# Kernel optimization log

Measured on AMD Instinct MI355X. Metric: run time of the kernel, lower is better.

Reference implementation:

```python
import jax, jax.numpy as jnp
import numpy as np

MAX_PT = 20; N_DIM = 2; OUT_SZ = MAX_PT * N_DIM + 2  # 42
FEAT = 512; HID = 512; B = 2048; NL = 32; H = 8; W = 8
SS_PROB = 0.1; BETA = 2.0


def setup_inputs() -> dict:
    key = jax.random.key(0)
    k = jax.random.split(key, 14)
    s = 0.02
    return {
        "img_features": jax.random.normal(k[0], (B, FEAT, H, W), jnp.float32),
        "ground_truth": jax.random.normal(k[1], (B, NL, MAX_PT * N_DIM), jnp.float32),
        "line_prob": jax.random.randint(k[2], (B, NL), 0, 2, jnp.int32),
        "sample_prob": jax.random.uniform(k[3], (NL, B), jnp.float32),
        "att_w": jax.random.normal(k[4], (FEAT + HID,), jnp.float32) * s,
        "att_b": jax.random.normal(k[5], (1,), jnp.float32) * s,
        "gru_w_ih": jax.random.normal(k[6], (3 * HID, FEAT + OUT_SZ), jnp.float32) * s,
        "gru_w_hh": jax.random.normal(k[7], (3 * HID, HID), jnp.float32) * s,
        "gru_b_ih": jax.random.normal(k[8], (3 * HID,), jnp.float32) * s,
        "gru_b_hh": jax.random.normal(k[9], (3 * HID,), jnp.float32) * s,
        "lin1_w": jax.random.normal(k[10], (512, HID), jnp.float32) * s,
        "lin1_b": jax.random.normal(k[11], (512,), jnp.float32) * s,
        "lin2_w": jax.random.normal(k[12], (OUT_SZ, 512), jnp.float32) * s,
        "lin2_b": jax.random.normal(k[13], (OUT_SZ,), jnp.float32) * s,
        "n_lines": NL,
    }


def reference(img_features, ground_truth, line_prob, sample_prob, att_w, att_b,
              gru_w_ih, gru_w_hh, gru_b_ih, gru_b_hh,
              lin1_w, lin1_b, lin2_w, lin2_b, n_lines):
    b, c, h, w = img_features.shape
    hw = h * w
    feat_flat = img_features.reshape(b, c, hw)                     # [B,C,HW]
    # attention branch uses a detached copy of the image features (and hidden)
    img_det = jax.lax.stop_gradient(feat_flat)
    img_logit = jnp.einsum('bcs,c->bs', img_det, att_w[:c])        # image half of 1x1 conv, constant over steps
    w_hid = att_w[c:]

    # scheduled-sampling GT input for step idx uses line idx-1; step 0 uses zeros (previous_output init)
    p = line_prob.astype(jnp.float32)[:, :, None]                  # [B,NL,1]
    ss_gt = jnp.concatenate([ground_truth, 1.0 - p, p], axis=-1)   # [B,NL,OUT]
    ss_gt = jnp.concatenate([jnp.zeros_like(ss_gt[:, :1]), ss_gt[:, :n_lines - 1]], axis=1)
    ss_gt = jnp.swapaxes(ss_gt, 0, 1)                              # [NL,B,OUT]
    use_prev = (sample_prob < SS_PROB).at[0].set(True)             # [NL,B]; step 0 always uses prev (zeros)

    def step(carry, xs):
        h_t, prev = carry
        gt_t, up_t = xs
        ss = jax.lax.stop_gradient(jnp.where(up_t[:, None], prev, gt_t))  # [B,OUT]
        hid_logit = jax.lax.stop_gradient(h_t) @ w_hid                    # [B] hidden half of 1x1 conv (detached)
        att = jax.nn.softmax(img_logit + hid_logit[:, None] + att_b[0], axis=1) * BETA  # [B,HW]
        att_feat = jnp.einsum('bcs,bs->bc', feat_flat, att)               # attention-pooled feature [B,C]
        x = jnp.concatenate([att_feat, ss], axis=1)                       # [B, C+OUT]
        # torch GRU cell: gates ordered r, z, n
        gi = x @ gru_w_ih.T + gru_b_ih
        gh = h_t @ gru_w_hh.T + gru_b_hh
        ir, iz, inn = jnp.split(gi, 3, axis=1)
        hr, hz, hn = jnp.split(gh, 3, axis=1)
        r = jax.nn.sigmoid(ir + hr)
        z = jax.nn.sigmoid(iz + hz)
        n = jnp.tanh(inn + r * hn)
        h_new = (1.0 - z) * n + z * h_t
        o = jax.nn.relu(h_new) @ lin1_w.T + lin1_b
        o = jax.nn.relu(o) @ lin2_w.T + lin2_b                            # [B,OUT]
        return (h_new, o), o

    h0 = jnp.zeros((b, gru_w_hh.shape[1]), img_features.dtype)
    o0 = jnp.zeros((b, lin2_w.shape[0]), img_features.dtype)
    _, outs = jax.lax.scan(step, (h0, o0), (ss_gt, use_prev))
    outs = jnp.swapaxes(outs, 0, 1)                                # [B,NL,OUT]
    npos = outs.shape[-1] - 2
    point_pos = outs[..., :npos]                                   # [B,NL,max_point*n_dim]
    line_out = jax.nn.softmax(outs[..., npos:].reshape(-1, 2), axis=1)  # [B*NL,2]
    return point_pos, line_out
```

## Files before the change

kernel.cpp:

```cpp
#include <hip/hip_runtime.h>
#include <hip/hip_bf16.h>
#include <cstdint>

#define B 2048
#define NL 32
#define FEAT 512
#define HID 512
#define HW 64
#define OUTSZ 42
#define G3 1536
#define LDIH 554
#define MB 16
#define NBLK (B/MB)
#define LDX 584
#define LDH 520
#define CPS 72
#define CHW 16384

typedef __bf16 bf16x8 __attribute__((ext_vector_type(8)));
typedef unsigned short u16x8 __attribute__((ext_vector_type(8)));
typedef float f32x4 __attribute__((ext_vector_type(4)));
typedef __hip_bfloat16 bf16_t;

#define MFMA(a,b,c) __builtin_amdgcn_mfma_f32_16x16x32_bf16(a,b,c,0,0,0)

#define WAITV4() asm volatile("s_waitcnt vmcnt(4)" ::: "memory")
#define PHASE_SYNC() do {                                            \
    asm volatile("s_waitcnt lgkmcnt(0)" ::: "memory");               \
    __builtin_amdgcn_s_barrier();                                    \
  } while (0)
#define PHASE_SYNC_V0() do {                                         \
    asm volatile("s_waitcnt vmcnt(0) lgkmcnt(0)" ::: "memory");      \
    __builtin_amdgcn_s_barrier();                                    \
  } while (0)

static __device__ __forceinline__ float sigmoidf_(float x){ return 1.f/(1.f+__expf(-x)); }

static __device__ __forceinline__ void gld16(const bf16_t* g, bf16_t* l){
  __builtin_amdgcn_global_load_lds(
      (const __attribute__((address_space(1))) void*)g,
      (__attribute__((address_space(3))) void*)l, 16, 0, 0);
}

__global__ __launch_bounds__(256) void prep4_kernel(
    const float* __restrict__ w_ih, const float* __restrict__ w_hh,
    const float* __restrict__ lin1_w, const float* __restrict__ lin2_w,
    const float* __restrict__ b_ih, const float* __restrict__ b_hh,
    bf16_t* __restrict__ sA, bf16_t* __restrict__ sB, bf16_t* __restrict__ sC,
    bf16_t* __restrict__ w_ssn, bf16_t* __restrict__ w_ih512b,
    float* __restrict__ bias_comb){
  const int NA = 54*CHW, NB2 = 16*CHW, NC2 = 2*CHW, NS = 512*64, NI = G3*512;
  const int total = NA+NB2+NC2+NS+NI+G3;
  for (int idx = blockIdx.x*256 + threadIdx.x; idx < total; idx += gridDim.x*256){
    int i = idx;
    if (i < NA){
      int c = i/CHW, r2 = i%CHW, rp = r2>>5, kk = r2&31, gq = kk>>3, e = kk&7;
      int k0 = c/3, g = c%3;
      int half = gq ^ ((rp>>1)&3);
      int orow = g*512 + rp;
      int k = k0*32 + half*8 + e;
      float v = (k < 512) ? w_hh[orow*512 + k]
              : ((k < 512+OUTSZ && g < 2) ? w_ih[(size_t)orow*LDIH + k] : 0.f);
      sA[i] = __float2bfloat16(v);
    } else if ((i -= NA) < NB2){
      int c = i/CHW, r2 = i%CHW, rp = r2>>5, kk = r2&31, gq = kk>>3, e = kk&7;
      int half = gq ^ ((rp>>1)&3);
      sB[i] = __float2bfloat16(lin1_w[rp*512 + c*32 + half*8 + e]);
    } else if ((i -= NB2) < NC2){
      int n = i/CHW, r2 = i%CHW, j = r2>>8, kk = r2&255, s = kk>>3, e = kk&7;
      int g = s ^ (j & 7);
      int k = n*256 + g*8 + e;
      float v = (j < OUTSZ) ? lin2_w[j*512 + k] : 0.f;
      sC[i] = __float2bfloat16(v);
    } else if ((i -= NC2) < NS){
      int j = i>>6, k = i&63;
      float v = (k < OUTSZ) ? w_ih[(size_t)(1024+j)*LDIH + 512 + k] : 0.f;
      w_ssn[i] = __float2bfloat16(v);
    } else if ((i -= NS) < NI){
      int r = i>>9, c = i&511;
      w_ih512b[i] = __float2bfloat16(w_ih[(size_t)r*LDIH + c]);
    } else {
      int j = i - NI;
      bias_comb[j] = b_ih[j] + (j < 1024 ? b_hh[j] : 0.f);
    }
  }
}

__global__ __launch_bounds__(256) void att_kernel(const float* __restrict__ feat,
                                                  const float* __restrict__ att_w,
                                                  bf16_t* __restrict__ att_feat){
  int b = blockIdx.x;
  const float* fb = feat + (size_t)b * FEAT * HW;
  __shared__ float part[4][64];
  __shared__ float attv[64];
  int t = threadIdx.x;
  int s = t & 63, q = t >> 6;
  float acc = 0.f;
  for (int c = q*128; c < q*128 + 128; ++c)
    acc = fmaf(fb[c*HW + s], att_w[c], acc);
  part[q][s] = acc;
  __syncthreads();
  if (t < 64){
    float v = part[0][t] + part[1][t] + part[2][t] + part[3][t];
    float m = v;
    for (int o = 32; o > 0; o >>= 1) m = fmaxf(m, __shfl_xor(m, o));
    float e = __expf(v - m);
    float ssum = e;
    for (int o = 32; o > 0; o >>= 1) ssum += __shfl_xor(ssum, o);
    attv[t] = e / ssum * 2.0f;
  }
  __syncthreads();
  for (int c = t; c < FEAT; c += 256){
    const float4* row = (const float4*)(fb + c*HW);
    float a2 = 0.f;
    #pragma unroll
    for (int k = 0; k < 16; ++k){
      float4 v4 = row[k];
      a2 = fmaf(v4.x, attv[k*4+0], a2);
      a2 = fmaf(v4.y, attv[k*4+1], a2);
      a2 = fmaf(v4.z, attv[k*4+2], a2);
      a2 = fmaf(v4.w, attv[k*4+3], a2);
    }
    att_feat[(size_t)b*FEAT + c] = __float2bfloat16(a2);
  }
}

__global__ __launch_bounds__(256) void gemm_mfma(const bf16_t* __restrict__ A,
                                                 const bf16_t* __restrict__ W,
                                                 const float* __restrict__ bias,
                                                 float* __restrict__ C,
                                                 int K, int lda, int ldw, int ldc){
  const int tid = threadIdx.x;
  const int w = tid >> 6, lane = tid & 63;
  const int r = lane & 15, half = lane >> 4;
  const int m_base = blockIdx.y * 64;
  const int n_base = blockIdx.x * 64 + w * 16;
  const bf16_t* Ap = A + (size_t)(m_base + r)*lda + half*8;
  const bf16_t* Wp = W + (size_t)(n_base + r)*ldw + half*8;
  f32x4 acc[4] = {};
  for (int k0 = 0; k0 < K; k0 += 32){
    bf16x8 bfrag = *(const bf16x8*)(Wp + k0);
    #pragma unroll
    for (int i = 0; i < 4; ++i){
      bf16x8 afrag = *(const bf16x8*)(Ap + (size_t)i*16*lda + k0);
      acc[i] = MFMA(afrag, bfrag, acc[i]);
    }
  }
  const float bv = bias ? bias[n_base + r] : 0.f;
  #pragma unroll
  for (int i = 0; i < 4; ++i)
    #pragma unroll
    for (int q = 0; q < 4; ++q)
      C[(size_t)(m_base + i*16 + half*4 + q)*ldc + n_base + r] = acc[i][q] + bv;
}

__global__ __launch_bounds__(512, 2) void mega13_kernel(
    const float* __restrict__ gi_base,
    const bf16_t* __restrict__ sA,
    const bf16_t* __restrict__ sB,
    const bf16_t* __restrict__ sC,
    const bf16_t* __restrict__ w_ssn,
    const float* __restrict__ lin1_b,
    const float* __restrict__ lin2_b,
    const float* __restrict__ b_hh,
    const float* __restrict__ gt,
    const int* __restrict__ line_prob,
    const float* __restrict__ sample_prob,
    float* __restrict__ out){
  __shared__ bf16_t ring[3*CHW];
  __shared__ bf16_t lds_x[MB][LDX];
  __shared__ bf16_t o1s[MB][LDH];
  const int tid = threadIdx.x;
  const int wv = tid >> 6, l = tid & 63;
  const int lr = l & 15, half = l >> 4;
  const int m0 = blockIdx.x * MB;
  const int colbase = wv * 64;
  const int rowoff = (colbase + lr)*32 + (half ^ ((lr >> 1) & 3))*8;

  for (int i = tid; i < MB*LDX/2; i += 512) ((uint32_t*)lds_x)[i] = 0u;

  float gir[4][4], giz[4][4], gin_[4][4];
  #pragma unroll
  for (int ti = 0; ti < 4; ++ti)
    #pragma unroll
    for (int q = 0; q < 4; ++q){
      const float* gp = gi_base + (size_t)(m0 + half*4 + q)*G3 + colbase + ti*16 + lr;
      gir[ti][q]  = gp[0];
      giz[ti][q]  = gp[512];
      gin_[ti][q] = gp[1024];
    }
  float bhn[4], lb1[4];
  #pragma unroll
  for (int ti = 0; ti < 4; ++ti){
    bhn[ti] = b_hh[1024 + colbase + ti*16 + lr];
    lb1[ti] = lin1_b[colbase + ti*16 + lr];
  }
  const int j3 = wv*16 + lr;
  const float b2c = (wv < 3 && j3 < OUTSZ) ? lin2_b[j3] : 0.f;
  bf16x8 sfr[4][2];
  #pragma unroll
  for (int ti = 0; ti < 4; ++ti)
    #pragma unroll
    for (int ks = 0; ks < 2; ++ks)
      sfr[ti][ks] = *(const bf16x8*)(w_ssn + (size_t)(colbase + ti*16 + lr)*64 + ks*32 + half*8);

  float hp[4][4] = {};

  auto issue = [&](uint32_t g){
    const bf16_t* src = sA;
    if (g < (uint32_t)NL*CPS){
      uint32_t c = g % CPS;
      src = (c < 54) ? sA + (size_t)c*CHW
          : (c < 70) ? sB + (size_t)(c-54)*CHW
                     : sC + (size_t)(c-70)*CHW;
    }
    const int off = wv*2048 + l*8;
    const bf16_t* s = src + off;
    bf16_t* dst = ring + (g % 3)*CHW + off;
    #pragma unroll
    for (int i = 0; i < 4; ++i)
      gld16(s + i*512, dst + i*512);
  };

  __syncthreads();
  uint32_t gc = 0;
  issue(0); issue(1);

  #pragma unroll 1
  for (int t = 0; t < NL; ++t){
    f32x4 accA[3][4] = {};
    #pragma unroll 1
    for (int k0 = 0; k0 < 18; ++k0){
      bf16x8 a = *(const bf16x8*)&lds_x[lr][k0*32 + half*8];
      #pragma unroll
      for (int g = 0; g < 3; ++g){
        WAITV4();
        issue(gc + 2);
        const bf16_t* S = ring + (gc % 3)*CHW;
        #pragma unroll
        for (int ti = 0; ti < 4; ++ti){
          bf16x8 bf = *(const bf16x8*)&S[rowoff + ti*512];
          accA[g][ti] = MFMA(a, bf, accA[g][ti]);
        }
        ++gc;
      }
    }

    f32x4 accS[4] = {};
    #pragma unroll
    for (int ks = 0; ks < 2; ++ks){
      bf16x8 a2 = *(const bf16x8*)&lds_x[lr][512 + ks*32 + half*8];
      #pragma unroll
      for (int ti = 0; ti < 4; ++ti)
        accS[ti] = MFMA(a2, sfr[ti][ks], accS[ti]);
    }
    PHASE_SYNC();

    #pragma unroll
    for (int ti = 0; ti < 4; ++ti)
      #pragma unroll
      for (int q = 0; q < 4; ++q){
        float ir = accA[0][ti][q] + gir[ti][q];
        float iz = accA[1][ti][q] + giz[ti][q];
        float hn = accA[2][ti][q] + bhn[ti];
        float gn = gin_[ti][q] + accS[ti][q];
        float r = sigmoidf_(ir);
        float z = sigmoidf_(iz);
        float n = tanhf(gn + r*hn);
        float hv = (1.f - z)*n + z*hp[ti][q];
        hp[ti][q] = hv;
        lds_x[half*4 + q][colbase + ti*16 + lr] = __float2bfloat16(hv);
      }
    PHASE_SYNC();

    f32x4 accB[4] = {};
    #pragma unroll 1
    for (int cb = 0; cb < 16; ++cb){
      WAITV4();
      issue(gc + 2);
      union { u16x8 u; bf16x8 b; } va;
      va.u = *(const u16x8*)&lds_x[lr][cb*32 + half*8];
      #pragma unroll
      for (int e = 0; e < 8; ++e)
        if (va.u[e] & 0x8000) va.u[e] = 0;
      const bf16_t* S = ring + (gc % 3)*CHW;
      #pragma unroll
      for (int ti = 0; ti < 4; ++ti){
        bf16x8 bf = *(const bf16x8*)&S[rowoff + ti*512];
        accB[ti] = MFMA(va.b, bf, accB[ti]);
      }
      ++gc;
    }
    #pragma unroll
    for (int ti = 0; ti < 4; ++ti)
      #pragma unroll
      for (int q = 0; q < 4; ++q)
        o1s[half*4 + q][colbase + ti*16 + lr] =
            __float2bfloat16(fmaxf(accB[ti][q] + lb1[ti], 0.f));
    PHASE_SYNC_V0();

    f32x4 accC = {};
    #pragma unroll
    for (int n = 0; n < 2; ++n){
      if (wv < 3){
        const bf16_t* S = ring + (gc % 3)*CHW;
        #pragma unroll
        for (int k0 = 0; k0 < 8; ++k0){
          bf16x8 a = *(const bf16x8*)&o1s[lr][(n*8 + k0)*32 + half*8];
          int sg = (k0*4 + half) ^ (j3 & 7);
          bf16x8 bf = *(const bf16x8*)&S[j3*256 + sg*8];
          accC = MFMA(a, bf, accC);
        }
      }
      ++gc;
    }
    if (wv < 3){
      #pragma unroll
      for (int q = 0; q < 4; ++q){
        float val = accC[q] + b2c;
        int row = half*4 + q;
        int bm = m0 + row;
        if (j3 < 40){
          out[((size_t)bm*NL + t)*40 + j3] = val;
        } else if (j3 < 42){
          float other = __shfl_xor(val, 1);
          float mx = fmaxf(val, other);
          float e0 = __expf(val - mx), e1 = __expf(other - mx);
          out[(size_t)B*NL*40 + ((size_t)bm*NL + t)*2 + (j3 - 40)] = e0/(e0 + e1);
        }
        if (t + 1 < NL && j3 < OUTSZ){
          bool up = sample_prob[(size_t)(t+1)*B + bm] < 0.1f;
          float gtv;
          if (j3 < 40) gtv = gt[((size_t)bm*NL + t)*40 + j3];
          else {
            float pv = (float)line_prob[bm*NL + t];
            gtv = (j3 == 40) ? 1.f - pv : pv;
          }
          lds_x[row][512 + j3] = __float2bfloat16(up ? val : gtv);
        }
      }
    }
    PHASE_SYNC();
    issue(gc);
    issue(gc + 1);
  }
}

extern "C" void kernel_launch(void* const* d_in, const int* in_sizes, int n_in,
                              void* d_out, int out_size, void* d_ws, size_t ws_size,
                              hipStream_t stream) {
  const float* img         = (const float*)d_in[0];
  const float* gt          = (const float*)d_in[1];
  const int*   line_prob   = (const int*)d_in[2];
  const float* sample_prob = (const float*)d_in[3];
  const float* att_w       = (const float*)d_in[4];
  const float* w_ih        = (const float*)d_in[6];
  const float* w_hh        = (const float*)d_in[7];
  const float* b_ih        = (const float*)d_in[8];
  const float* b_hh        = (const float*)d_in[9];
  const float* lin1_w      = (const float*)d_in[10];
  const float* lin1_b      = (const float*)d_in[11];
  const float* lin2_w      = (const float*)d_in[12];
  const float* lin2_b      = (const float*)d_in[13];
  float* out = (float*)d_out;

  char* p = (char*)d_ws;
  auto alloc = [&](size_t bytes){ void* q = p; p += (bytes + 255) & ~(size_t)255; return q; };
  float*  gi_base   = (float*)alloc((size_t)B*G3*4);
  bf16_t* att_bf    = (bf16_t*)alloc((size_t)B*FEAT*2);
  bf16_t* sA        = (bf16_t*)alloc((size_t)54*CHW*2);
  bf16_t* sB        = (bf16_t*)alloc((size_t)16*CHW*2);
  bf16_t* sC        = (bf16_t*)alloc((size_t)2*CHW*2);
  bf16_t* w_ssn     = (bf16_t*)alloc((size_t)512*64*2);
  bf16_t* w_ih512b  = (bf16_t*)alloc((size_t)G3*512*2);
  float*  bias_comb = (float*)alloc((size_t)G3*4);

  prep4_kernel<<<4096, 256, 0, stream>>>(w_ih, w_hh, lin1_w, lin2_w, b_ih, b_hh,
                                         sA, sB, sC, w_ssn, w_ih512b, bias_comb);
  att_kernel<<<B, 256, 0, stream>>>(img, att_w, att_bf);
  gemm_mfma<<<dim3(G3/64, B/64), 256, 0, stream>>>(att_bf, w_ih512b, bias_comb, gi_base,
                                                   512, 512, 512, G3);
  mega13_kernel<<<NBLK, 512, 0, stream>>>(gi_base, sA, sB, sC, w_ssn, lin1_b, lin2_b,
                                          b_hh, gt, line_prob, sample_prob, out);
}
```

Measured before the change: 1.117 ms.

## Split weight-streaming ring into half-size chunks with deeper six-slot prefetch

Weight chunks streamed into LDS are halved (16 K-columns instead of 32), and the ring grows from 3 to 6 slots with prefetch depth 5 instead of 2. The LDS footprint of the ring stays the same. Each half-chunk feeds only the lanes holding that K half, while the other lanes multiply against a zero region in lds_x, so every half-chunk costs a full MFMA set. The aim is finer-grained, deeper overlap of global-to-LDS loads, paid for with twice as many MFMAs and extra wait points in the recurrent GEMMs.

Result: slower. 1.921 ms (+71.9%).

```diff
diff --git a/kernel.cpp b/kernel.cpp
--- a/kernel.cpp
+++ b/kernel.cpp
@@ -14,8 +14,8 @@
 #define NBLK (B/MB)
 #define LDX 584
 #define LDH 520
-#define CPS 72
-#define CHW 16384
+#define CPS 144
+#define CW 8192
 
 typedef __bf16 bf16x8 __attribute__((ext_vector_type(8)));
 typedef unsigned short u16x8 __attribute__((ext_vector_type(8)));
@@ -24,7 +24,7 @@
 
 #define MFMA(a,b,c) __builtin_amdgcn_mfma_f32_16x16x32_bf16(a,b,c,0,0,0)
 
-#define WAITV4() asm volatile("s_waitcnt vmcnt(4)" ::: "memory")
+#define WAITV8() asm volatile("s_waitcnt vmcnt(8)" ::: "memory")
 #define PHASE_SYNC() do {                                            \
     asm volatile("s_waitcnt lgkmcnt(0)" ::: "memory");               \
     __builtin_amdgcn_s_barrier();                                    \
@@ -42,34 +42,36 @@
       (__attribute__((address_space(3))) void*)l, 16, 0, 0);
 }
 
-__global__ __launch_bounds__(256) void prep4_kernel(
+__global__ __launch_bounds__(256) void prep5_kernel(
     const float* __restrict__ w_ih, const float* __restrict__ w_hh,
     const float* __restrict__ lin1_w, const float* __restrict__ lin2_w,
     const float* __restrict__ b_ih, const float* __restrict__ b_hh,
     bf16_t* __restrict__ sA, bf16_t* __restrict__ sB, bf16_t* __restrict__ sC,
     bf16_t* __restrict__ w_ssn, bf16_t* __restrict__ w_ih512b,
     float* __restrict__ bias_comb){
-  const int NA = 54*CHW, NB2 = 16*CHW, NC2 = 2*CHW, NS = 512*64, NI = G3*512;
+  const int NA = 108*CW, NB2 = 32*CW, NC2 = 4*CW, NS = 512*64, NI = G3*512;
   const int total = NA+NB2+NC2+NS+NI+G3;
   for (int idx = blockIdx.x*256 + threadIdx.x; idx < total; idx += gridDim.x*256){
     int i = idx;
     if (i < NA){
-      int c = i/CHW, r2 = i%CHW, rp = r2>>5, kk = r2&31, gq = kk>>3, e = kk&7;
-      int k0 = c/3, g = c%3;
-      int half = gq ^ ((rp>>1)&3);
+      int c = i/CW, r2 = i%CW, rp = r2>>4, kk = r2&15, gq = kk>>3, e = kk&7;
+      int k0 = c/6, rem = c%6, g = rem>>1, kh = rem&1;
+      int f = gq ^ ((rp>>2)&1);
+      int k = k0*32 + kh*16 + f*8 + e;
       int orow = g*512 + rp;
-      int k = k0*32 + half*8 + e;
       float v = (k < 512) ? w_hh[orow*512 + k]
               : ((k < 512+OUTSZ && g < 2) ? w_ih[(size_t)orow*LDIH + k] : 0.f);
       sA[i] = __float2bfloat16(v);
     } else if ((i -= NA) < NB2){
-      int c = i/CHW, r2 = i%CHW, rp = r2>>5, kk = r2&31, gq = kk>>3, e = kk&7;
-      int half = gq ^ ((rp>>1)&3);
-      sB[i] = __float2bfloat16(lin1_w[rp*512 + c*32 + half*8 + e]);
+      int c = i/CW, r2 = i%CW, rp = r2>>4, kk = r2&15, gq = kk>>3, e = kk&7;
+      int kb = c>>1, kh = c&1;
+      int f = gq ^ ((rp>>2)&1);
+      int k = kb*32 + kh*16 + f*8 + e;
+      sB[i] = __float2bfloat16(lin1_w[rp*512 + k]);
     } else if ((i -= NB2) < NC2){
-      int n = i/CHW, r2 = i%CHW, j = r2>>8, kk = r2&255, s = kk>>3, e = kk&7;
-      int g = s ^ (j & 7);
-      int k = n*256 + g*8 + e;
+      int n = i/CW, r2 = i%CW, j = r2>>7, kk = r2&127, gq2 = kk>>3, e = kk&7;
+      int sG = gq2 ^ (j & 7);
+      int k = n*128 + sG*8 + e;
       float v = (j < OUTSZ) ? lin2_w[j*512 + k] : 0.f;
       sC[i] = __float2bfloat16(v);
     } else if ((i -= NC2) < NS){
@@ -154,7 +156,7 @@
       C[(size_t)(m_base + i*16 + half*4 + q)*ldc + n_base + r] = acc[i][q] + bv;
 }
 
-__global__ __launch_bounds__(512, 2) void mega13_kernel(
+__global__ __launch_bounds__(512, 2) void mega14_kernel(
     const float* __restrict__ gi_base,
     const bf16_t* __restrict__ sA,
     const bf16_t* __restrict__ sB,
@@ -167,7 +169,7 @@
     const int* __restrict__ line_prob,
     const float* __restrict__ sample_prob,
     float* __restrict__ out){
-  __shared__ bf16_t ring[3*CHW];
+  __shared__ bf16_t ring[6*CW];
   __shared__ bf16_t lds_x[MB][LDX];
   __shared__ bf16_t o1s[MB][LDH];
   const int tid = threadIdx.x;
@@ -175,9 +177,16 @@
   const int lr = l & 15, half = l >> 4;
   const int m0 = blockIdx.x * MB;
   const int colbase = wv * 64;
-  const int rowoff = (colbase + lr)*32 + (half ^ ((lr >> 1) & 3))*8;
+  const bool lowk = (half < 2);
 
   for (int i = tid; i < MB*LDX/2; i += 512) ((uint32_t*)lds_x)[i] = 0u;
+
+  const int p8 = ((half & 1) ^ ((lr >> 2) & 1)) * 8;
+  int rdoff[4];
+  #pragma unroll
+  for (int ti = 0; ti < 4; ++ti)
+    rdoff[ti] = (colbase + ti*16 + lr)*16 + p8;
+  const bf16_t* zptr = &lds_x[0][560];
 
   float gir[4][4], giz[4][4], gin_[4][4];
   #pragma unroll
@@ -210,21 +219,20 @@
     const bf16_t* src = sA;
     if (g < (uint32_t)NL*CPS){
       uint32_t c = g % CPS;
-      src = (c < 54) ? sA + (size_t)c*CHW
-          : (c < 70) ? sB + (size_t)(c-54)*CHW
-                     : sC + (size_t)(c-70)*CHW;
-    }
-    const int off = wv*2048 + l*8;
+      src = (c < 108) ? sA + (size_t)c*CW
+          : (c < 140) ? sB + (size_t)(c-108)*CW
+                      : sC + (size_t)(c-140)*CW;
+    }
+    const int off = wv*1024 + l*8;
     const bf16_t* s = src + off;
-    bf16_t* dst = ring + (g % 3)*CHW + off;
-    #pragma unroll
-    for (int i = 0; i < 4; ++i)
-      gld16(s + i*512, dst + i*512);
+    bf16_t* dst = ring + (g % 6)*CW + off;
+    gld16(s, dst);
+    gld16(s + 512, dst + 512);
   };
 
   __syncthreads();
   uint32_t gc = 0;
-  issue(0); issue(1);
+  issue(0); issue(1); issue(2); issue(3); issue(4);
 
   #pragma unroll 1
   for (int t = 0; t < NL; ++t){
@@ -234,15 +242,20 @@
       bf16x8 a = *(const bf16x8*)&lds_x[lr][k0*32 + half*8];
       #pragma unroll
       for (int g = 0; g < 3; ++g){
-        WAITV4();
-        issue(gc + 2);
-        const bf16_t* S = ring + (gc % 3)*CHW;
         #pragma unroll
-        for (int ti = 0; ti < 4; ++ti){
-          bf16x8 bf = *(const bf16x8*)&S[rowoff + ti*512];
-          accA[g][ti] = MFMA(a, bf, accA[g][ti]);
+        for (int kh = 0; kh < 2; ++kh){
+          WAITV8();
+          issue(gc + 5);
+          const bf16_t* S = ring + (gc % 6)*CW;
+          const bool act = (kh == 0) ? lowk : !lowk;
+          #pragma unroll
+          for (int ti = 0; ti < 4; ++ti){
+            const bf16_t* bp = act ? (S + rdoff[ti]) : zptr;
+            bf16x8 bf = *(const bf16x8*)bp;
+            accA[g][ti] = MFMA(a, bf, accA[g][ti]);
+          }
+          ++gc;
         }
-        ++gc;
       }
     }
 
@@ -275,21 +288,26 @@
 
     f32x4 accB[4] = {};
     #pragma unroll 1
-    for (int cb = 0; cb < 16; ++cb){
-      WAITV4();
-      issue(gc + 2);
+    for (int kb = 0; kb < 16; ++kb){
       union { u16x8 u; bf16x8 b; } va;
-      va.u = *(const u16x8*)&lds_x[lr][cb*32 + half*8];
+      va.u = *(const u16x8*)&lds_x[lr][kb*32 + half*8];
       #pragma unroll
       for (int e = 0; e < 8; ++e)
         if (va.u[e] & 0x8000) va.u[e] = 0;
-      const bf16_t* S = ring + (gc % 3)*CHW;
-      #pragma unroll
-      for (int ti = 0; ti < 4; ++ti){
-        bf16x8 bf = *(const bf16x8*)&S[rowoff + ti*512];
-        accB[ti] = MFMA(va.b, bf, accB[ti]);
+      #pragma unroll
+      for (int kh = 0; kh < 2; ++kh){
+        WAITV8();
+        issue(gc + 5);
+        const bf16_t* S = ring + (gc % 6)*CW;
+        const bool act = (kh == 0) ? lowk : !lowk;
+        #pragma unroll
+        for (int ti = 0; ti < 4; ++ti){
+          const bf16_t* bp = act ? (S + rdoff[ti]) : zptr;
+          bf16x8 bf = *(const bf16x8*)bp;
+          accB[ti] = MFMA(va.b, bf, accB[ti]);
+        }
+        ++gc;
       }
-      ++gc;
     }
     #pragma unroll
     for (int ti = 0; ti < 4; ++ti)
@@ -301,14 +319,14 @@
 
     f32x4 accC = {};
     #pragma unroll
-    for (int n = 0; n < 2; ++n){
+    for (int n = 0; n < 4; ++n){
       if (wv < 3){
-        const bf16_t* S = ring + (gc % 3)*CHW;
+        const bf16_t* S = ring + (gc % 6)*CW;
         #pragma unroll
-        for (int k0 = 0; k0 < 8; ++k0){
-          bf16x8 a = *(const bf16x8*)&o1s[lr][(n*8 + k0)*32 + half*8];
-          int sg = (k0*4 + half) ^ (j3 & 7);
-          bf16x8 bf = *(const bf16x8*)&S[j3*256 + sg*8];
+        for (int k0l = 0; k0l < 4; ++k0l){
+          bf16x8 a = *(const bf16x8*)&o1s[lr][(n*4 + k0l)*32 + half*8];
+          int sg = (k0l*4 + half) ^ (j3 & 7);
+          bf16x8 bf = *(const bf16x8*)&S[j3*128 + sg*8];
           accC = MFMA(a, bf, accC);
         }
       }
@@ -341,8 +359,7 @@
       }
     }
     PHASE_SYNC();
-    issue(gc);
-    issue(gc + 1);
+    issue(gc + 1); issue(gc + 2); issue(gc + 3); issue(gc + 4);
   }
 }
 
@@ -368,18 +385,18 @@
   auto alloc = [&](size_t bytes){ void* q = p; p += (bytes + 255) & ~(size_t)255; return q; };
   float*  gi_base   = (float*)alloc((size_t)B*G3*4);
   bf16_t* att_bf    = (bf16_t*)alloc((size_t)B*FEAT*2);
-  bf16_t* sA        = (bf16_t*)alloc((size_t)54*CHW*2);
-  bf16_t* sB        = (bf16_t*)alloc((size_t)16*CHW*2);
-  bf16_t* sC        = (bf16_t*)alloc((size_t)2*CHW*2);
+  bf16_t* sA        = (bf16_t*)alloc((size_t)108*CW*2);
+  bf16_t* sB        = (bf16_t*)alloc((size_t)32*CW*2);
+  bf16_t* sC        = (bf16_t*)alloc((size_t)4*CW*2);
   bf16_t* w_ssn     = (bf16_t*)alloc((size_t)512*64*2);
   bf16_t* w_ih512b  = (bf16_t*)alloc((size_t)G3*512*2);
   float*  bias_comb = (float*)alloc((size_t)G3*4);
 
-  prep4_kernel<<<4096, 256, 0, stream>>>(w_ih, w_hh, lin1_w, lin2_w, b_ih, b_hh,
+  prep5_kernel<<<4096, 256, 0, stream>>>(w_ih, w_hh, lin1_w, lin2_w, b_ih, b_hh,
                                          sA, sB, sC, w_ssn, w_ih512b, bias_comb);
   att_kernel<<<B, 256, 0, stream>>>(img, att_w, att_bf);
   gemm_mfma<<<dim3(G3/64, B/64), 256, 0, stream>>>(att_bf, w_ih512b, bias_comb, gi_base,
                                                    512, 512, 512, G3);
-  mega13_kernel<<<NBLK, 512, 0, stream>>>(gi_base, sA, sB, sC, w_ssn, lin1_b, lin2_b,
+  mega14_kernel<<<NBLK, 512, 0, stream>>>(gi_base, sA, sB, sC, w_ssn, lin1_b, lin2_b,
                                           b_hh, gt, line_prob, sample_prob, out);
 }
```
